# Kernel tuning notes

Hardware: AMD Instinct MI355X
Metric: run time of the kernel (lower is better)

The kernel has to match this reference:

```python
import jax, jax.numpy as jnp
import numpy as np

N = 48          # nagents
D = 16          # ndims
K = 2           # edge_type (excluding type-0 'no edge')
H = 256         # MLP hidden units
B = 32          # batch
PRED = 8        # pred_steps


def setup_inputs() -> dict:
    key = jax.random.key(0)
    ks = jax.random.split(key, 12)
    # fully-connected edges without self loops (fc_matrix)
    src_np, tgt_np = np.nonzero(np.ones((N, N), np.int8) - np.eye(N, dtype=np.int8))
    src_idx = jnp.asarray(src_np, jnp.int32)   # [E]
    tgt_idx = jnp.asarray(tgt_np, jnp.int32)   # [E]
    E = src_idx.shape[0]                       # 2256

    time_segs = jax.random.normal(ks[0], (B, 1, N, D), jnp.float32)
    types = jax.random.randint(ks[1], (B, E), 0, K + 1)
    edge_types = jax.nn.one_hot(types, K + 1, dtype=jnp.float32)  # [B,E,K+1]

    def glorot(k, shape, fan_in):
        return jax.random.normal(k, shape, jnp.float32) * (1.0 / np.sqrt(fan_in))

    enc_W1 = glorot(ks[2], (K, 2 * D, H), 2 * D)
    enc_b1 = jnp.zeros((K, H), jnp.float32)
    enc_W2 = glorot(ks[3], (K, H, H), H)
    enc_b2 = jnp.zeros((K, H), jnp.float32)
    dec_W1 = glorot(ks[4], (D + H, H), D + H)
    dec_b1 = jnp.zeros((H,), jnp.float32)
    dec_W2 = glorot(ks[5], (H, H), H)
    dec_b2 = jnp.zeros((H,), jnp.float32)
    out_W = glorot(ks[6], (H, D), H)
    out_b = jnp.zeros((D,), jnp.float32)

    return dict(time_segs=time_segs, edge_types=edge_types,
                src_idx=src_idx, tgt_idx=tgt_idx,
                enc_W1=enc_W1, enc_b1=enc_b1, enc_W2=enc_W2, enc_b2=enc_b2,
                dec_W1=dec_W1, dec_b1=dec_b1, dec_W2=dec_W2, dec_b2=dec_b2,
                out_W=out_W, out_b=out_b)


def reference(time_segs, edge_types, src_idx, tgt_idx,
              enc_W1, enc_b1, enc_W2, enc_b2,
              dec_W1, dec_b1, dec_W2, dec_b2,
              out_W, out_b):
    # time_segs: [B, 1, N, D]; edge_types: [B, E, K+1]
    b = time_segs.shape[0]
    # transpose to [B, N, T, D]; time_seg_len == 1 so conv1d is identity and
    # each step consumes only the latest state.
    state = jnp.transpose(time_segs, (0, 2, 1, 3))[:, :, -1, :]  # [B, N, D]
    et = edge_types[:, :, 1:, None]                              # [B, E, K, 1]

    outs = []
    for _ in range(PRED):
        # gather node pairs -> per-edge message [B, E, 2D]
        edge_msg = jnp.concatenate([state[:, src_idx], state[:, tgt_idx]], axis=-1)
        # per-edge-type MLP encode: [B, E, K, H]
        h = jax.nn.relu(jnp.einsum('bef,kfh->bekh', edge_msg, enc_W1) + enc_b1)
        h = jax.nn.relu(jnp.einsum('bekh,khg->bekg', h, enc_W2) + enc_b2)
        # masked reduce over edge types -> [B, E, H]
        agg = jnp.sum(h * et, axis=2)
        # scatter-aggregate edge messages to target nodes -> [B, N, H]
        node_msg = jnp.zeros((b, N, H), agg.dtype).at[:, tgt_idx].add(agg)
        # node decode
        node_in = jnp.concatenate([state, node_msg], axis=-1)    # [B, N, D+H]
        d = jax.nn.relu(node_in @ dec_W1 + dec_b1)
        d = jax.nn.relu(d @ dec_W2 + dec_b2)
        # residual update
        state = state + d @ out_W + out_b                        # [B, N, D]
        outs.append(state)
    return jnp.stack(outs, axis=1)  # [B, PRED, N, D]
```

## Files before the change

### kernel.cpp

```cpp
#include <hip/hip_runtime.h>

#define NN    48
#define DD    16
#define HH    256
#define EE    2256
#define BB    32
#define NPRED 8
#define LSTR  56
#define PQS   1040
#define TMAX  7
#define ROWB  80
#define APL   (TMAX*16*ROWB)

typedef __attribute__((ext_vector_type(4))) float f32x4;
typedef __attribute__((ext_vector_type(8))) short short8;

__device__ __forceinline__ float bf2f(unsigned short h) {
    union { unsigned u; float f; } v; v.u = ((unsigned)h) << 16; return v.f;
}
__device__ __forceinline__ unsigned short f2bf(float x) {
    union { float f; unsigned u; } v; v.f = x;
    unsigned r = v.u + 0x7fffu + ((v.u >> 16) & 1u);
    return (unsigned short)(r >> 16);
}
__device__ __forceinline__ unsigned perm_hi16(unsigned xB, unsigned xA, unsigned sel) {
    unsigned d;
    asm("v_perm_b32 %0, %1, %2, %3" : "=v"(d) : "v"(xB), "v"(xA), "s"(sel));
    return d;
}
struct Split3 { unsigned d0, d1, d2; };
__device__ __forceinline__ Split3 split2(float u0, float u1, unsigned sel)
{
    union F { float f; unsigned u; };
    Split3 o;
    F x0, x1; x0.f = u0; x1.f = u1;
    o.d0 = perm_hi16(x1.u, x0.u, sel);
    F h0a, h0b; h0a.u = x0.u & 0xffff0000u; h0b.u = x1.u & 0xffff0000u;
    F e0a, e0b; e0a.f = u0 - h0a.f; e0b.f = u1 - h0b.f;
    o.d1 = perm_hi16(e0b.u, e0a.u, sel);
    F h1a, h1b; h1a.u = e0a.u & 0xffff0000u; h1b.u = e0b.u & 0xffff0000u;
    F e1a, e1b; e1a.f = e0a.f - h1a.f; e1b.f = e0b.f - h1b.f;
    o.d2 = perm_hi16(e1b.u, e1a.u, sel);
    return o;
}
union PackA { unsigned u[4]; short8 s; };

__global__ __launch_bounds__(256) void k_setup(
    const float* __restrict__ time_segs,
    const float* __restrict__ edge_types,
    const float* __restrict__ W1,
    const float* __restrict__ W2,
    const float* __restrict__ b1,
    float* __restrict__ state,
    float* __restrict__ W1T,
    unsigned short* __restrict__ W2f,
    float* __restrict__ PQ,
    int* __restrict__ lists,
    int* __restrict__ counts)
{
    const int tid = blockIdx.x * 256 + threadIdx.x;
    const int NT = 384*256;
    for (int i = tid; i < BB*NN*DD; i += NT)
        state[i] = time_segs[i];
    for (int i = tid; i < 2*HH*32; i += NT) {
        const int t = i >> 13, r = i & 8191, h = r >> 5, f = r & 31;
        W1T[i] = W1[(t*32 + f)*HH + h];
    }
    for (int i = tid; i < 2*8*16*64*8; i += NT) {
        const int j  = i & 7, l = (i >> 3) & 63, nt = (i >> 9) & 15;
        const int kt = (i >> 13) & 7, t = (i >> 16) & 1;
        const int k = kt*32 + ((l >> 4) << 3) + j;
        const int n = nt*16 + (l & 15);
        const float w = W2[((size_t)t*HH + k)*HH + n];
        const unsigned short h0 = f2bf(w);  const float r1 = w  - bf2f(h0);
        const unsigned short h1 = f2bf(r1); const float r2 = r1 - bf2f(h1);
        const unsigned short h2 = f2bf(r2);
        const size_t rest = (size_t)kt*8192 + nt*512 + l*8 + j;
        W2f[(size_t)(t*3+0)*65536 + rest] = h0;
        W2f[(size_t)(t*3+1)*65536 + rest] = h1;
        W2f[(size_t)(t*3+2)*65536 + rest] = h2;
    }
    for (int i = tid; i < BB*NN*1024; i += NT) {
        const int c  = i & 255;
        const int pq = (i >> 8) & 1;
        const int t  = (i >> 9) & 1;
        const int nb = i >> 10;
        float v = pq ? b1[t*HH + c] : 0.f;
        #pragma unroll
        for (int f = 0; f < DD; ++f)
            v = fmaf(time_segs[nb*DD + f], W1[(t*32 + pq*16 + f)*HH + c], v);
        PQ[(size_t)nb*PQS + (i & 1023)] = v;
    }
    if (tid < BB*NN) {
        const int b = tid / NN;
        const int n = tid % NN;
        int* lst = lists + tid * LSTR;
        int c = 0;
        for (int s = 0; s < NN; ++s) {
            if (s == n) continue;
            const int e = s * 47 + (n > s ? n - 1 : n);
            if (edge_types[((size_t)b*EE + e)*3 + 1] > 0.5f) lst[c++] = s;
        }
        const int c1 = c;
        for (int s = 0; s < NN; ++s) {
            if (s == n) continue;
            const int e = s * 47 + (n > s ? n - 1 : n);
            if (edge_types[((size_t)b*EE + e)*3 + 2] > 0.5f) lst[c++] = s;
        }
        counts[tid*2 + 0] = c1;
        counts[tid*2 + 1] = c - c1;
        for (int i = c; i < LSTR; ++i) lst[i] = 0;
    }
}

__global__ __launch_bounds__(256, 4) void k_enc(
    const int*   __restrict__ lists,
    const int*   __restrict__ counts,
    const float* __restrict__ PQ,
    const unsigned short* __restrict__ W2f,
    const float* __restrict__ b2,
    float* __restrict__ node_msg)
{
    const int lb     = (blockIdx.x & 7)*192 + (blockIdx.x >> 3);
    const int b      = lb / 48;
    const int rem    = lb % 48;
    const int pair   = rem >> 1;
    const int nthalf = rem & 1;
    const int n0     = pair * 2;
    const int tid    = threadIdx.x;
    const int lane   = tid & 63, wave = tid >> 6;
    const unsigned PSEL = 0x07060302u;

    __shared__ __align__(16) char Apl[3*APL];
    __shared__ int rowinfo_s[TMAX*16];

    const int c00 = counts[(b*NN + n0    )*2 + 0];
    const int c10 = counts[(b*NN + n0    )*2 + 1];
    const int c01 = counts[(b*NN + n0 + 1)*2 + 0];
    const int c11 = counts[(b*NN + n0 + 1)*2 + 1];
    const int tA  = c00 + c01, tB = c10 + c11;
    const int tAt = (tA + 15) >> 4, tBt = (tB + 15) >> 4;
    const int tiles = tAt + tBt;
    const int rows  = tiles*16;

    if (tid < TMAX*16) {
        const int r = tid;
        int g = 4, src = 0;
        if (r < tAt*16) {
            if (r < c00)     { src = lists[(b*NN + n0    )*LSTR + r];        g = 0; }
            else if (r < tA) { src = lists[(b*NN + n0 + 1)*LSTR + (r - c00)]; g = 1; }
        } else if (r < rows) {
            const int s = r - tAt*16;
            if (s < c10)     { src = lists[(b*NN + n0    )*LSTR + c00 + s];        g = 2; }
            else if (s < tB) { src = lists[(b*NN + n0 + 1)*LSTR + c01 + (s - c10)]; g = 3; }
        }
        rowinfo_s[r] = src | (g << 8);
    }
    __syncthreads();

    f32x4 acc[TMAX][2];
    #pragma unroll
    for (int q = 0; q < TMAX; ++q) {
        acc[q][0] = (f32x4){0.f, 0.f, 0.f, 0.f};
        acc[q][1] = (f32x4){0.f, 0.f, 0.f, 0.f};
    }

    const float* PQb = PQ + (size_t)b*NN*PQS;
    const int ntb  = nthalf*8 + wave*2;
    const int abase = (lane & 15)*ROWB + (lane >> 4)*16;

    #pragma unroll 1
    for (int kt = 0; kt < 8; ++kt) {
        #pragma unroll
        for (int pass = 0; pass < 2; ++pass) {
            const int item = tid + pass*256;
            const int row  = item >> 2, quad = item & 3;
            if (row < rows) {
                const int info = rowinfo_s[row];
                const int src  = info & 255;
                const int nd   = (info >> 8) & 1;
                const int tq   = (row >= tAt*16) ? 1 : 0;
                const int cols = kt*32 + quad*8;
                const float* pr = PQb + src*PQS      + tq*512 +       cols;
                const float* qr = PQb + (n0+nd)*PQS  + tq*512 + 256 + cols;
                const float4 Pa = *(const float4*)pr, Pb = *(const float4*)(pr+4);
                const float4 Qa = *(const float4*)qr, Qb = *(const float4*)(qr+4);
                const float u0 = fmaxf(Pa.x + Qa.x, 0.f);
                const float u1 = fmaxf(Pa.y + Qa.y, 0.f);
                const float u2 = fmaxf(Pa.z + Qa.z, 0.f);
                const float u3 = fmaxf(Pa.w + Qa.w, 0.f);
                const float u4 = fmaxf(Pb.x + Qb.x, 0.f);
                const float u5 = fmaxf(Pb.y + Qb.y, 0.f);
                const float u6 = fmaxf(Pb.z + Qb.z, 0.f);
                const float u7 = fmaxf(Pb.w + Qb.w, 0.f);
                const Split3 s0 = split2(u0, u1, PSEL);
                const Split3 s1 = split2(u2, u3, PSEL);
                const Split3 s2 = split2(u4, u5, PSEL);
                const Split3 s3 = split2(u6, u7, PSEL);
                char* w = Apl + row*ROWB + quad*16;
                PackA A0, A1, A2;
                A0.u[0]=s0.d0; A0.u[1]=s1.d0; A0.u[2]=s2.d0; A0.u[3]=s3.d0;
                A1.u[0]=s0.d1; A1.u[1]=s1.d1; A1.u[2]=s2.d1; A1.u[3]=s3.d1;
                A2.u[0]=s0.d2; A2.u[1]=s1.d2; A2.u[2]=s2.d2; A2.u[3]=s3.d2;
                *(short8*)(w)         = A0.s;
                *(short8*)(w + APL)   = A1.s;
                *(short8*)(w + 2*APL) = A2.s;
            }
        }
        __syncthreads();

        #pragma unroll
        for (int sec = 0; sec < 2; ++sec) {
            const int qlo = sec ? tAt : 0;
            const int qhi = sec ? tiles : tAt;
            if (qlo >= qhi) continue;
            short8 Bf[2][3];
            #pragma unroll
            for (int i = 0; i < 2; ++i)
                #pragma unroll
                for (int p = 0; p < 3; ++p)
                    Bf[i][p] = *(const short8*)(W2f + ((size_t)(sec*3+p)*65536
                                 + (size_t)kt*8192 + (size_t)(ntb + i)*512 + (size_t)lane*8));
            #pragma unroll
            for (int q = 0; q < TMAX; ++q) {
                if (q >= qlo && q < qhi) {
                    short8 Af[3];
                    const char* ap = Apl + q*16*ROWB + abase;
                    #pragma unroll
                    for (int p = 0; p < 3; ++p)
                        Af[p] = *(const short8*)(ap + p*APL);
                    #pragma unroll
                    for (int i = 0; i < 2; ++i) {
                        f32x4 a = acc[q][i];
                        a = __builtin_amdgcn_mfma_f32_16x16x32_bf16(Af[2], Bf[i][0], a, 0, 0, 0);
                        a = __builtin_amdgcn_mfma_f32_16x16x32_bf16(Af[1], Bf[i][1], a, 0, 0, 0);
                        a = __builtin_amdgcn_mfma_f32_16x16x32_bf16(Af[0], Bf[i][2], a, 0, 0, 0);
                        a = __builtin_amdgcn_mfma_f32_16x16x32_bf16(Af[1], Bf[i][0], a, 0, 0, 0);
                        a = __builtin_amdgcn_mfma_f32_16x16x32_bf16(Af[0], Bf[i][1], a, 0, 0, 0);
                        a = __builtin_amdgcn_mfma_f32_16x16x32_bf16(Af[0], Bf[i][0], a, 0, 0, 0);
                        acc[q][i] = a;
                    }
                }
            }
        }
        __syncthreads();
    }

    float b2v[2][2];
    #pragma unroll
    for (int t = 0; t < 2; ++t)
        #pragma unroll
        for (int i = 0; i < 2; ++i)
            b2v[t][i] = b2[t*HH + (ntb + i)*16 + (lane & 15)];

    float p0[2], p1[2];
    p0[0] = p0[1] = p1[0] = p1[1] = 0.f;
    #pragma unroll
    for (int q = 0; q < TMAX; ++q) {
        if (q < tiles) {
            const bool secB = (q >= tAt);
            int gv[4];
            #pragma unroll
            for (int rr = 0; rr < 4; ++rr)
                gv[rr] = rowinfo_s[q*16 + (lane >> 4)*4 + rr] >> 8;
            #pragma unroll
            for (int i = 0; i < 2; ++i) {
                const float bias = secB ? b2v[1][i] : b2v[0][i];
                #pragma unroll
                for (int rr = 0; rr < 4; ++rr) {
                    const float v = fmaxf(acc[q][i][rr] + bias, 0.f);
                    const bool valid = gv[rr] < 4;
                    p0[i] += (valid && !(gv[rr] & 1)) ? v : 0.f;
                    p1[i] += (valid &&  (gv[rr] & 1)) ? v : 0.f;
                }
            }
        }
    }
    #pragma unroll
    for (int i = 0; i < 2; ++i) {
        float v0 = p0[i], v1 = p1[i];
        v0 += __shfl_xor(v0, 16); v0 += __shfl_xor(v0, 32);
        v1 += __shfl_xor(v1, 16); v1 += __shfl_xor(v1, 32);
        if ((lane >> 4) == 0) {
            node_msg[((size_t)(b*NN + n0  ))*HH + (ntb + i)*16 + lane] = v0;
            node_msg[((size_t)(b*NN + n0+1))*HH + (ntb + i)*16 + lane] = v1;
        }
    }
}

__global__ __launch_bounds__(256, 2) void k_dec(
    float* __restrict__ state,
    const float* __restrict__ nm,
    const float* __restrict__ W1, const float* __restrict__ b1,
    const float* __restrict__ W2, const float* __restrict__ b2,
    const float* __restrict__ W3, const float* __restrict__ b3,
    const float* __restrict__ eW1T,
    const float* __restrict__ eb1,
    float* __restrict__ PQ,
    float* __restrict__ out, int step)
{
    const int lb   = (blockIdx.x & 7)*48 + (blockIdx.x >> 3);
    const int b    = lb / 12;
    const int row0 = (lb % 12) * 4;
    const int c    = threadIdx.x;

    __shared__ float in_s[4][272];
    __shared__ float d1s[4][HH];
    __shared__ float stn[4][DD];

    for (int i = c; i < 4*272; i += 256) {
        const int m = i / 272, k = i % 272;
        const int r = row0 + m;
        in_s[m][k] = (k < DD)
            ? state[((size_t)b*NN + r)*DD + k]
            : nm[((size_t)b*NN + r)*HH + (k - DD)];
    }
    __syncthreads();

    float a0[4];
    {
        const float bb = b1[c];
        #pragma unroll
        for (int m = 0; m < 4; ++m) a0[m] = bb;
        #pragma unroll 2
        for (int k4 = 0; k4 < 68; ++k4) {
            const float* wr = W1 + (k4*4)*HH;
            const float w0=wr[c], w1_=wr[HH+c], w2_=wr[2*HH+c], w3=wr[3*HH+c];
            #pragma unroll
            for (int m = 0; m < 4; ++m) {
                const float4 h = *(const float4*)&in_s[m][k4*4];
                a0[m] = fmaf(h.x,w0, fmaf(h.y,w1_, fmaf(h.z,w2_, fmaf(h.w,w3, a0[m]))));
            }
        }
        #pragma unroll
        for (int m = 0; m < 4; ++m) d1s[m][c] = fmaxf(a0[m], 0.f);
    }
    __syncthreads();
    {
        const float bb = b2[c];
        #pragma unroll
        for (int m = 0; m < 4; ++m) a0[m] = bb;
        #pragma unroll 2
        for (int k4 = 0; k4 < 64; ++k4) {
            const float* wr = W2 + (k4*4)*HH;
            const float w0=wr[c], w1_=wr[HH+c], w2_=wr[2*HH+c], w3=wr[3*HH+c];
            #pragma unroll
            for (int m = 0; m < 4; ++m) {
                const float4 h = *(const float4*)&d1s[m][k4*4];
                a0[m] = fmaf(h.x,w0, fmaf(h.y,w1_, fmaf(h.z,w2_, fmaf(h.w,w3, a0[m]))));
            }
        }
        __syncthreads();
        #pragma unroll
        for (int m = 0; m < 4; ++m) in_s[m][c] = fmaxf(a0[m], 0.f);
    }
    __syncthreads();
    if (c < 64) {
        const int m = c >> 4, cc = c & 15;
        float a = b3[cc];
        #pragma unroll 4
        for (int k4 = 0; k4 < 64; ++k4) {
            const float4 h = *(const float4*)&in_s[m][k4*4];
            a += h.x*W3[(k4*4+0)*16+cc] + h.y*W3[(k4*4+1)*16+cc]
               + h.z*W3[(k4*4+2)*16+cc] + h.w*W3[(k4*4+3)*16+cc];
        }
        const int r = row0 + m;
        const float v = state[((size_t)b*NN + r)*DD + cc] + a;
        state[((size_t)b*NN + r)*DD + cc] = v;
        out[(((size_t)b*NPRED + step)*NN + r)*DD + cc] = v;
        stn[m][cc] = v;
    }
    __syncthreads();
    float4 sm[4][4];
    #pragma unroll
    for (int m = 0; m < 4; ++m)
        #pragma unroll
        for (int f4 = 0; f4 < 4; ++f4)
            sm[m][f4] = *(const float4*)&stn[m][f4*4];
    #pragma unroll
    for (int k = 0; k < 4; ++k) {
        const int combo = c + 256*k;
        const int cc = combo & 255;
        const int pq = (combo >> 8) & 1;
        const int t  = combo >> 9;
        const float* wc = eW1T + ((size_t)t*HH + cc)*32 + pq*16;
        float4 w[4];
        #pragma unroll
        for (int f4 = 0; f4 < 4; ++f4) w[f4] = ((const float4*)wc)[f4];
        const float bias = pq ? eb1[t*HH + cc] : 0.f;
        #pragma unroll
        for (int m = 0; m < 4; ++m) {
            float v = bias;
            #pragma unroll
            for (int f4 = 0; f4 < 4; ++f4) {
                const float4 s = sm[m][f4];
                v = fmaf(s.x,w[f4].x, fmaf(s.y,w[f4].y, fmaf(s.z,w[f4].z, fmaf(s.w,w[f4].w, v))));
            }
            PQ[(size_t)(b*NN + row0 + m)*PQS + t*512 + pq*256 + cc] = v;
        }
    }
}

extern "C" void kernel_launch(void* const* d_in, const int* in_sizes, int n_in,
                              void* d_out, int out_size, void* d_ws, size_t ws_size,
                              hipStream_t stream)
{
    const float* time_segs  = (const float*)d_in[0];
    const float* edge_types = (const float*)d_in[1];
    const float* enc_W1 = (const float*)d_in[4];
    const float* enc_b1 = (const float*)d_in[5];
    const float* enc_W2 = (const float*)d_in[6];
    const float* enc_b2 = (const float*)d_in[7];
    const float* dec_W1 = (const float*)d_in[8];
    const float* dec_b1 = (const float*)d_in[9];
    const float* dec_W2 = (const float*)d_in[10];
    const float* dec_b2 = (const float*)d_in[11];
    const float* out_W  = (const float*)d_in[12];
    const float* out_b  = (const float*)d_in[13];
    float* out = (float*)d_out;

    float* state    = (float*)d_ws;
    float* node_msg = state + BB*NN*DD;
    float* W1T      = node_msg + BB*NN*HH;
    unsigned short* W2f = (unsigned short*)(W1T + 2*HH*32);
    int*   lists    = (int*)(W2f + 2*3*65536);
    int*   counts   = lists + BB*NN*LSTR;
    float* PQ       = (float*)(counts + BB*NN*2);

    k_setup<<<384, 256, 0, stream>>>(time_segs, edge_types, enc_W1, enc_W2,
                                     enc_b1, state, W1T, W2f, PQ, lists, counts);
    for (int stp = 0; stp < NPRED; ++stp) {
        k_enc<<<BB*NN, 256, 0, stream>>>(lists, counts, PQ, W2f,
                                         enc_b2, node_msg);
        k_dec<<<BB*12, 256, 0, stream>>>(state, node_msg,
                                         dec_W1, dec_b1, dec_W2, dec_b2,
                                         out_W, out_b, W1T, enc_b1, PQ, out, stp);
    }
}
```

Before: 628.1 us.

## Merge encoder half-blocks into 512-thread blocks and give decoder blocks six rows

The encoder kernel now runs one 512-thread block per node pair instead of two 256-thread blocks that each built the same A tile and handled half the output columns. The gather/ReLU/bf16 staging of the edge rows is therefore done once per pair rather than twice. The decoder moves from 4 rows per block across 384 blocks to 6 rows per block across 256 blocks, so each weight load is reused over more rows. The trade-off is fewer blocks per launch and higher per-block register and LDS pressure, with launch bounds of (512,4) limiting registers.

```diff
diff --git a/kernel.cpp b/kernel.cpp
--- a/kernel.cpp
+++ b/kernel.cpp
@@ -113,7 +113,27 @@
     }
 }
 
-__global__ __launch_bounds__(256, 4) void k_enc(
+#define MFMA6(Ax, Bi, a)                                                       \
+    a = __builtin_amdgcn_mfma_f32_16x16x32_bf16(Ax[2], Bi[0], a, 0, 0, 0);     \
+    a = __builtin_amdgcn_mfma_f32_16x16x32_bf16(Ax[1], Bi[1], a, 0, 0, 0);     \
+    a = __builtin_amdgcn_mfma_f32_16x16x32_bf16(Ax[0], Bi[2], a, 0, 0, 0);     \
+    a = __builtin_amdgcn_mfma_f32_16x16x32_bf16(Ax[1], Bi[0], a, 0, 0, 0);     \
+    a = __builtin_amdgcn_mfma_f32_16x16x32_bf16(Ax[0], Bi[1], a, 0, 0, 0);     \
+    a = __builtin_amdgcn_mfma_f32_16x16x32_bf16(Ax[0], Bi[0], a, 0, 0, 0);
+
+#define MM1(qq)                                                                \
+    {                                                                          \
+        short8 Af[3];                                                          \
+        const char* ap = Apl + (qq)*16*ROWB + abase;                           \
+        _Pragma("unroll")                                                      \
+        for (int p = 0; p < 3; ++p) Af[p] = *(const short8*)(ap + p*APL);      \
+        f32x4 x0 = acc[qq][0], x1 = acc[qq][1];                                \
+        MFMA6(Af, Bf[0], x0)                                                   \
+        MFMA6(Af, Bf[1], x1)                                                   \
+        acc[qq][0] = x0; acc[qq][1] = x1;                                      \
+    }
+
+__global__ __launch_bounds__(512, 4) void k_enc(
     const int*   __restrict__ lists,
     const int*   __restrict__ counts,
     const float* __restrict__ PQ,
@@ -121,14 +141,12 @@
     const float* __restrict__ b2,
     float* __restrict__ node_msg)
 {
-    const int lb     = (blockIdx.x & 7)*192 + (blockIdx.x >> 3);
-    const int b      = lb / 48;
-    const int rem    = lb % 48;
-    const int pair   = rem >> 1;
-    const int nthalf = rem & 1;
-    const int n0     = pair * 2;
-    const int tid    = threadIdx.x;
-    const int lane   = tid & 63, wave = tid >> 6;
+    const int lb   = (blockIdx.x & 7)*96 + (blockIdx.x >> 3);
+    const int b    = lb / 24;
+    const int pair = lb % 24;
+    const int n0   = pair * 2;
+    const int tid  = threadIdx.x;
+    const int lane = tid & 63, wave = tid >> 6;
     const unsigned PSEL = 0x07060302u;
 
     __shared__ __align__(16) char Apl[3*APL];
@@ -166,15 +184,13 @@
     }
 
     const float* PQb = PQ + (size_t)b*NN*PQS;
-    const int ntb  = nthalf*8 + wave*2;
+    const int ntb  = wave*2;
     const int abase = (lane & 15)*ROWB + (lane >> 4)*16;
 
     #pragma unroll 1
     for (int kt = 0; kt < 8; ++kt) {
-        #pragma unroll
-        for (int pass = 0; pass < 2; ++pass) {
-            const int item = tid + pass*256;
-            const int row  = item >> 2, quad = item & 3;
+        {
+            const int row  = tid >> 2, quad = tid & 3;
             if (row < rows) {
                 const int info = rowinfo_s[row];
                 const int src  = info & 255;
@@ -223,24 +239,7 @@
                                  + (size_t)kt*8192 + (size_t)(ntb + i)*512 + (size_t)lane*8));
             #pragma unroll
             for (int q = 0; q < TMAX; ++q) {
-                if (q >= qlo && q < qhi) {
-                    short8 Af[3];
-                    const char* ap = Apl + q*16*ROWB + abase;
-                    #pragma unroll
-                    for (int p = 0; p < 3; ++p)
-                        Af[p] = *(const short8*)(ap + p*APL);
-                    #pragma unroll
-                    for (int i = 0; i < 2; ++i) {
-                        f32x4 a = acc[q][i];
-                        a = __builtin_amdgcn_mfma_f32_16x16x32_bf16(Af[2], Bf[i][0], a, 0, 0, 0);
-                        a = __builtin_amdgcn_mfma_f32_16x16x32_bf16(Af[1], Bf[i][1], a, 0, 0, 0);
-                        a = __builtin_amdgcn_mfma_f32_16x16x32_bf16(Af[0], Bf[i][2], a, 0, 0, 0);
-                        a = __builtin_amdgcn_mfma_f32_16x16x32_bf16(Af[1], Bf[i][0], a, 0, 0, 0);
-                        a = __builtin_amdgcn_mfma_f32_16x16x32_bf16(Af[0], Bf[i][1], a, 0, 0, 0);
-                        a = __builtin_amdgcn_mfma_f32_16x16x32_bf16(Af[0], Bf[i][0], a, 0, 0, 0);
-                        acc[q][i] = a;
-                    }
-                }
+                if (q >= qlo && q < qhi) { MM1(q) }
             }
         }
         __syncthreads();
@@ -299,16 +298,16 @@
     float* __restrict__ PQ,
     float* __restrict__ out, int step)
 {
-    const int lb   = (blockIdx.x & 7)*48 + (blockIdx.x >> 3);
-    const int b    = lb / 12;
-    const int row0 = (lb % 12) * 4;
+    const int lb   = (blockIdx.x & 7)*32 + (blockIdx.x >> 3);
+    const int b    = lb / 8;
+    const int row0 = (lb % 8) * 6;
     const int c    = threadIdx.x;
 
-    __shared__ float in_s[4][272];
-    __shared__ float d1s[4][HH];
-    __shared__ float stn[4][DD];
-
-    for (int i = c; i < 4*272; i += 256) {
+    __shared__ float in_s[6][272];
+    __shared__ float d1s[6][HH];
+    __shared__ float stn[6][DD];
+
+    for (int i = c; i < 6*272; i += 256) {
         const int m = i / 272, k = i % 272;
         const int r = row0 + m;
         in_s[m][k] = (k < DD)
@@ -317,45 +316,45 @@
     }
     __syncthreads();
 
-    float a0[4];
+    float a0[6];
     {
         const float bb = b1[c];
         #pragma unroll
-        for (int m = 0; m < 4; ++m) a0[m] = bb;
+        for (int m = 0; m < 6; ++m) a0[m] = bb;
         #pragma unroll 2
         for (int k4 = 0; k4 < 68; ++k4) {
             const float* wr = W1 + (k4*4)*HH;
             const float w0=wr[c], w1_=wr[HH+c], w2_=wr[2*HH+c], w3=wr[3*HH+c];
             #pragma unroll
-            for (int m = 0; m < 4; ++m) {
+            for (int m = 0; m < 6; ++m) {
                 const float4 h = *(const float4*)&in_s[m][k4*4];
                 a0[m] = fmaf(h.x,w0, fmaf(h.y,w1_, fmaf(h.z,w2_, fmaf(h.w,w3, a0[m]))));
             }
         }
         #pragma unroll
-        for (int m = 0; m < 4; ++m) d1s[m][c] = fmaxf(a0[m], 0.f);
+        for (int m = 0; m < 6; ++m) d1s[m][c] = fmaxf(a0[m], 0.f);
     }
     __syncthreads();
     {
         const float bb = b2[c];
         #pragma unroll
-        for (int m = 0; m < 4; ++m) a0[m] = bb;
+        for (int m = 0; m < 6; ++m) a0[m] = bb;
         #pragma unroll 2
         for (int k4 = 0; k4 < 64; ++k4) {
             const float* wr = W2 + (k4*4)*HH;
             const float w0=wr[c], w1_=wr[HH+c], w2_=wr[2*HH+c], w3=wr[3*HH+c];
             #pragma unroll
-            for (int m = 0; m < 4; ++m) {
+            for (int m = 0; m < 6; ++m) {
                 const float4 h = *(const float4*)&d1s[m][k4*4];
                 a0[m] = fmaf(h.x,w0, fmaf(h.y,w1_, fmaf(h.z,w2_, fmaf(h.w,w3, a0[m]))));
             }
         }
         __syncthreads();
         #pragma unroll
-        for (int m = 0; m < 4; ++m) in_s[m][c] = fmaxf(a0[m], 0.f);
+        for (int m = 0; m < 6; ++m) in_s[m][c] = fmaxf(a0[m], 0.f);
     }
     __syncthreads();
-    if (c < 64) {
+    if (c < 96) {
         const int m = c >> 4, cc = c & 15;
         float a = b3[cc];
         #pragma unroll 4
@@ -371,9 +370,9 @@
         stn[m][cc] = v;
     }
     __syncthreads();
-    float4 sm[4][4];
-    #pragma unroll
-    for (int m = 0; m < 4; ++m)
+    float4 sm[6][4];
+    #pragma unroll
+    for (int m = 0; m < 6; ++m)
         #pragma unroll
         for (int f4 = 0; f4 < 4; ++f4)
             sm[m][f4] = *(const float4*)&stn[m][f4*4];
@@ -389,7 +388,7 @@
         for (int f4 = 0; f4 < 4; ++f4) w[f4] = ((const float4*)wc)[f4];
         const float bias = pq ? eb1[t*HH + cc] : 0.f;
         #pragma unroll
-        for (int m = 0; m < 4; ++m) {
+        for (int m = 0; m < 6; ++m) {
             float v = bias;
             #pragma unroll
             for (int f4 = 0; f4 < 4; ++f4) {
@@ -430,10 +429,10 @@
     k_setup<<<384, 256, 0, stream>>>(time_segs, edge_types, enc_W1, enc_W2,
                                      enc_b1, state, W1T, W2f, PQ, lists, counts);
     for (int stp = 0; stp < NPRED; ++stp) {
-        k_enc<<<BB*NN, 256, 0, stream>>>(lists, counts, PQ, W2f,
+        k_enc<<<BB*24, 512, 0, stream>>>(lists, counts, PQ, W2f,
                                          enc_b2, node_msg);
-        k_dec<<<BB*12, 256, 0, stream>>>(state, node_msg,
-                                         dec_W1, dec_b1, dec_W2, dec_b2,
-                                         out_W, out_b, W1T, enc_b1, PQ, out, stp);
-    }
-}
+        k_dec<<<BB*8, 256, 0, stream>>>(state, node_msg,
+                                        dec_W1, dec_b1, dec_W2, dec_b2,
+                                        out_W, out_b, W1T, enc_b1, PQ, out, stp);
+    }
+}
```

After: 594.5 us. -5.4%, faster.
